# Performance work log

Measured on AMD Instinct MI355X. Metric: run time of the kernel, lower is better.

The kernel has to match this reference:

```python
import jax, jax.numpy as jnp
import numpy as np

N, E, NFEAT, HID, HEADS, NCLASS = 100000, 1600000, 256, 64, 1, 32


def gat_conv(x, src, dst, W, a_src, a_dst, b, H, C, concat):
    n = x.shape[0]
    h = (x @ W).reshape(n, H, C)                      # [N,H,C]
    a_s = (h * a_src).sum(-1)                          # [N,H]
    a_d = (h * a_dst).sum(-1)                          # [N,H]
    e = jax.nn.leaky_relu(a_s[src] + a_d[dst], 0.2)    # [E,H]
    emax = jax.ops.segment_max(e, dst, num_segments=n)
    emax = jnp.where(jnp.isfinite(emax), emax, 0.0)
    ex = jnp.exp(e - emax[dst])
    denom = jax.ops.segment_sum(ex, dst, num_segments=n)
    alpha = ex / (denom[dst] + 1e-16)                  # segment softmax over in-edges of dst
    msg = h[src] * alpha[:, :, None]                   # [E,H,C]
    out = jax.ops.segment_sum(msg, dst, num_segments=n)
    out = out.reshape(n, H * C) if concat else out.mean(axis=1)
    return out + b


def setup_inputs() -> dict:
    key = jax.random.key(0)
    ks = jax.random.split(key, 14)
    x = jax.random.normal(ks[0], (N, NFEAT), dtype=jnp.float32)
    edge_index = jax.random.randint(ks[1], (2, E), 0, N, dtype=jnp.int64)
    s = 0.05
    return {
        'x': x, 'edge_index': edge_index,
        'W1': jax.random.normal(ks[2], (NFEAT, HEADS * HID), jnp.float32) * s,
        'as1': jax.random.normal(ks[3], (HEADS, HID), jnp.float32) * s,
        'ad1': jax.random.normal(ks[4], (HEADS, HID), jnp.float32) * s,
        'b1': jnp.zeros((HEADS * HID,), jnp.float32),
        'W2': jax.random.normal(ks[5], (HEADS * HID, HEADS * HID), jnp.float32) * s,
        'as2': jax.random.normal(ks[6], (HEADS, HID), jnp.float32) * s,
        'ad2': jax.random.normal(ks[7], (HEADS, HID), jnp.float32) * s,
        'b2': jnp.zeros((HEADS * HID,), jnp.float32),
        'W3': jax.random.normal(ks[8], (HEADS * HID, HEADS * NCLASS), jnp.float32) * s,
        'as3': jax.random.normal(ks[9], (HEADS, NCLASS), jnp.float32) * s,
        'ad3': jax.random.normal(ks[10], (HEADS, NCLASS), jnp.float32) * s,
        'b3': jnp.zeros((NCLASS,), jnp.float32),
    }


def reference(x, edge_index, W1, as1, ad1, b1, W2, as2, ad2, b2, W3, as3, ad3, b3):
    # add self loops (PyG GATConv add_self_loops=True)
    loop = jnp.arange(N, dtype=edge_index.dtype)
    src = jnp.concatenate([edge_index[0], loop])
    dst = jnp.concatenate([edge_index[1], loop])
    out = jax.nn.leaky_relu(gat_conv(x, src, dst, W1, as1, ad1, b1, HEADS, HID, True), 0.01)
    out = jax.nn.leaky_relu(gat_conv(out, src, dst, W2, as2, ad2, b2, HEADS, HID, True), 0.01)
    out = gat_conv(out, src, dst, W3, as3, ad3, b3, HEADS, NCLASS, False)
    return out
```

## Files before the change

kernel.cpp:

```cpp
#include <hip/hip_runtime.h>

#define NN 100000
#define NE 1600000
#define NF 256
#define HD 64
#define NC 32

#define BKS 8
#define NBK ((NN + 255) >> 8)
#define CHUNK 4096
#define NBLK ((NE + CHUNK - 1) / CHUNK)

__device__ __forceinline__ float lrelu02(float x) { return fmaxf(x, 0.2f * x); }


__global__ __launch_bounds__(256) void bucket_hist(const int* __restrict__ dst, int* __restrict__ gcnt) {
    __shared__ int hist[NBK];
    int tid = threadIdx.x;
    for (int i = tid; i < NBK; i += 256) hist[i] = 0;
    __syncthreads();
    int base = blockIdx.x * CHUNK;
    #pragma unroll
    for (int k = 0; k < CHUNK / 256; k++) {
        int i = base + k * 256 + tid;
        if (i < NE) atomicAdd(&hist[dst[i] >> BKS], 1);
    }
    __syncthreads();
    for (int i = tid; i < NBK; i += 256) if (hist[i]) atomicAdd(&gcnt[i], hist[i]);
}

__global__ void bucket_scan(const int* __restrict__ gcnt, int* __restrict__ gbase, int* __restrict__ gcur) {
    __shared__ int sh[512];
    int tid = threadIdx.x;
    int v = (tid < NBK) ? gcnt[tid] : 0;
    sh[tid] = v;
    __syncthreads();
    for (int d = 1; d < 512; d <<= 1) {
        int t = (tid >= d) ? sh[tid - d] : 0;
        __syncthreads();
        sh[tid] += t;
        __syncthreads();
    }
    if (tid < NBK) { int ex = sh[tid] - v; gbase[tid] = ex; gcur[tid] = ex; }
}

__global__ __launch_bounds__(256) void bin_edges(const int* __restrict__ src, const int* __restrict__ dst,
                                                 int* __restrict__ gcur, int2* __restrict__ ebuf) {
    __shared__ int hist[NBK];
    __shared__ int excl[NBK];
    __shared__ int runbase[NBK];
    __shared__ int ssum[256];
    __shared__ int2 sorted[CHUNK];
    int tid = threadIdx.x;
    int base = blockIdx.x * CHUNK;
    int n = NE - base; if (n > CHUNK) n = CHUNK;

    for (int i = tid; i < NBK; i += 256) hist[i] = 0;
    __syncthreads();

    int2 ed[CHUNK / 256];
    int bk[CHUNK / 256];
    #pragma unroll
    for (int k = 0; k < CHUNK / 256; k++) {
        int i = base + k * 256 + tid;
        if (i < NE) {
            ed[k] = make_int2(src[i], dst[i]);
            bk[k] = ed[k].y >> BKS;
            atomicAdd(&hist[bk[k]], 1);
        } else bk[k] = -1;
    }
    __syncthreads();
    int h0 = (2 * tid < NBK) ? hist[2 * tid] : 0;
    int h1 = (2 * tid + 1 < NBK) ? hist[2 * tid + 1] : 0;
    ssum[tid] = h0 + h1;
    __syncthreads();
    for (int d = 1; d < 256; d <<= 1) {
        int t = (tid >= d) ? ssum[tid - d] : 0;
        __syncthreads();
        ssum[tid] += t;
        __syncthreads();
    }
    int pref = ssum[tid] - (h0 + h1);
    if (2 * tid < NBK) excl[2 * tid] = pref;
    if (2 * tid + 1 < NBK) excl[2 * tid + 1] = pref + h0;
    for (int b = tid; b < NBK; b += 256) {
        int c = hist[b];
        runbase[b] = c ? atomicAdd(&gcur[b], c) : 0;
    }
    __syncthreads();
    #pragma unroll
    for (int k = 0; k < CHUNK / 256; k++) {
        if (bk[k] >= 0) {
            int r = atomicAdd(&excl[bk[k]], 1);
            sorted[r] = ed[k];
        }
    }
    __syncthreads();
    for (int i = tid; i < n; i += 256) {
        int2 e = sorted[i];
        int b = e.y >> BKS;
        int local_rank = i - (excl[b] - hist[b]);
        ebuf[runbase[b] + local_rank] = e;
    }
}

__global__ __launch_bounds__(256) void bucket_csr(const int2* __restrict__ ebuf, const int* __restrict__ gbase,
                                                  const int* __restrict__ gcnt,
                                                  int* __restrict__ offs, int* __restrict__ csr) {
    __shared__ int hist[256], cur[256], ssum[256];
    int b = blockIdx.x, tid = threadIdx.x;
    int ebeg = gbase[b], cnt = gcnt[b];
    int node0 = b << BKS;
    hist[tid] = 0;
    __syncthreads();
    for (int i = ebeg + tid; i < ebeg + cnt; i += 256)
        atomicAdd(&hist[ebuf[i].y & 255], 1);
    __syncthreads();
    int v = hist[tid];
    ssum[tid] = v;
    __syncthreads();
    for (int d = 1; d < 256; d <<= 1) {
        int t = (tid >= d) ? ssum[tid - d] : 0;
        __syncthreads();
        ssum[tid] += t;
        __syncthreads();
    }
    int ex = ebeg + ssum[tid] - v;
    cur[tid] = ex;
    int nnode = NN - node0; if (nnode > 256) nnode = 256;
    if (tid < nnode) offs[node0 + tid] = ex;
    if (b == NBK - 1 && tid == nnode - 1) offs[NN] = ebeg + cnt;
    __syncthreads();
    for (int i = ebeg + tid; i < ebeg + cnt; i += 256) {
        int2 e = ebuf[i];
        int pos = atomicAdd(&cur[e.y & 255], 1);
        csr[pos] = e.x;
    }
}


template <int CIN, int COUT, int CG>
__global__ __launch_bounds__(256) void rb_gemm(const float* __restrict__ in, const float* __restrict__ W,
                                               const float* __restrict__ a_s, const float* __restrict__ a_d,
                                               float* __restrict__ h, float* __restrict__ asv,
                                               float* __restrict__ adv) {
    const int KC  = 32;
    const int NG  = 256 / CG;
    const int BN  = NG * 4;
    const int BNP = BN + 4;
    __shared__ float xsT[KC * BNP];
    __shared__ float Wl[KC * COUT];
    int tid = threadIdx.x;
    int cg = tid % CG;
    int ng = tid / CG;
    int c0 = cg * 8;
    int n0base = blockIdx.x * BN;

    float4 a0[4], a1[4];
    #pragma unroll
    for (int i = 0; i < 4; i++) { a0[i] = make_float4(0,0,0,0); a1[i] = make_float4(0,0,0,0); }

    for (int k0 = 0; k0 < CIN; k0 += KC) {
        __syncthreads();
        const int XF4 = BN * KC / 4;
        #pragma unroll
        for (int f = tid; f < XF4; f += 256) {
            int n = f >> 3;
            int q = f & 7;
            int gn = n0base + n;
            float4 v = make_float4(0,0,0,0);
            if (gn < NN) v = *(const float4*)&in[(size_t)gn * CIN + k0 + q * 4];
            xsT[(q * 4 + 0) * BNP + n] = v.x;
            xsT[(q * 4 + 1) * BNP + n] = v.y;
            xsT[(q * 4 + 2) * BNP + n] = v.z;
            xsT[(q * 4 + 3) * BNP + n] = v.w;
        }
        #pragma unroll
        for (int f = tid; f < KC * COUT / 4; f += 256)
            *(float4*)&Wl[f * 4] = *(const float4*)&W[(size_t)k0 * COUT + f * 4];
        __syncthreads();
        #pragma unroll 4
        for (int k = 0; k < KC; k++) {
            float4 xv = *(float4*)&xsT[k * BNP + ng * 4];
            float4 w0 = *(float4*)&Wl[k * COUT + c0];
            float4 w1 = *(float4*)&Wl[k * COUT + c0 + 4];
            #pragma unroll
            for (int i = 0; i < 4; i++) {
                float xc = (i == 0) ? xv.x : (i == 1) ? xv.y : (i == 2) ? xv.z : xv.w;
                a0[i].x += xc * w0.x; a0[i].y += xc * w0.y; a0[i].z += xc * w0.z; a0[i].w += xc * w0.w;
                a1[i].x += xc * w1.x; a1[i].y += xc * w1.y; a1[i].z += xc * w1.z; a1[i].w += xc * w1.w;
            }
        }
    }
    float4 As0 = *(const float4*)&a_s[c0];
    float4 As1 = *(const float4*)&a_s[c0 + 4];
    float4 Ad0 = *(const float4*)&a_d[c0];
    float4 Ad1 = *(const float4*)&a_d[c0 + 4];
    #pragma unroll
    for (int i = 0; i < 4; i++) {
        int n = n0base + ng * 4 + i;
        if (n < NN) {
            *(float4*)&h[(size_t)n * COUT + c0] = a0[i];
            *(float4*)&h[(size_t)n * COUT + c0 + 4] = a1[i];
        }
        float vs = a0[i].x * As0.x + a0[i].y * As0.y + a0[i].z * As0.z + a0[i].w * As0.w
                 + a1[i].x * As1.x + a1[i].y * As1.y + a1[i].z * As1.z + a1[i].w * As1.w;
        float vd = a0[i].x * Ad0.x + a0[i].y * Ad0.y + a0[i].z * Ad0.z + a0[i].w * Ad0.w
                 + a1[i].x * Ad1.x + a1[i].y * Ad1.y + a1[i].z * Ad1.z + a1[i].w * Ad1.w;
        #pragma unroll
        for (int off = 1; off < CG; off <<= 1) { vs += __shfl_xor(vs, off); vd += __shfl_xor(vd, off); }
        if (cg == 0 && n < NN) { asv[n] = vs; adv[n] = vd; }
    }
}


template <int C, bool ACT>
__global__ __launch_bounds__(256) void gat_agg(const float* __restrict__ h, const float* __restrict__ asv,
                                               const float* __restrict__ adv, const int* __restrict__ offs,
                                               const int* __restrict__ csr,
                                               const float* __restrict__ bias, float* __restrict__ out) {
    const int LPR = C / 4;
    const int G = 64 / LPR;
    const float4* h4 = (const float4*)h;
    int lane = threadIdx.x & 63;
    int v = blockIdx.x * 4 + (threadIdx.x >> 6);
    int beg = offs[v], end = offs[v + 1];
    int g = lane / LPR, r = lane % LPR;
    float adv_v = adv[v];

    float4 acc = {0.f, 0.f, 0.f, 0.f};
    float dsum = 0.f;
    #pragma unroll 4
    for (int e = beg + g; e < end; e += G) {
        int s = csr[e];
        float ww = __expf(lrelu02(asv[s] + adv_v));
        float4 hv = h4[(size_t)s * LPR + r];
        dsum += ww;
        acc.x += ww * hv.x; acc.y += ww * hv.y; acc.z += ww * hv.z; acc.w += ww * hv.w;
    }
    #pragma unroll
    for (int off = LPR; off < 64; off <<= 1) {
        acc.x += __shfl_xor(acc.x, off);
        acc.y += __shfl_xor(acc.y, off);
        acc.z += __shfl_xor(acc.z, off);
        acc.w += __shfl_xor(acc.w, off);
        dsum += __shfl_xor(dsum, off);
    }
    if (g == 0) {
        float selfw = __expf(lrelu02(asv[v] + adv_v));
        float4 hs = h4[(size_t)v * LPR + r];
        acc.x += selfw * hs.x; acc.y += selfw * hs.y;
        acc.z += selfw * hs.z; acc.w += selfw * hs.w;
        dsum += selfw;
        float inv = 1.f / (dsum + 1e-16f);
        float4 bb = ((const float4*)bias)[r];
        float4 o;
        o.x = acc.x * inv + bb.x; o.y = acc.y * inv + bb.y;
        o.z = acc.z * inv + bb.z; o.w = acc.w * inv + bb.w;
        if (ACT) {
            o.x = fmaxf(o.x, 0.01f * o.x); o.y = fmaxf(o.y, 0.01f * o.y);
            o.z = fmaxf(o.z, 0.01f * o.z); o.w = fmaxf(o.w, 0.01f * o.w);
        }
        ((float4*)out)[(size_t)v * LPR + r] = o;
    }
}


extern "C" void kernel_launch(void* const* d_in, const int* in_sizes, int n_in,
                              void* d_out, int out_size, void* d_ws, size_t ws_size,
                              hipStream_t stream) {
    const float* x   = (const float*)d_in[0];
    const int*   ei  = (const int*)d_in[1];
    const float* W1  = (const float*)d_in[2];
    const float* as1 = (const float*)d_in[3];
    const float* ad1 = (const float*)d_in[4];
    const float* b1  = (const float*)d_in[5];
    const float* W2  = (const float*)d_in[6];
    const float* as2 = (const float*)d_in[7];
    const float* ad2 = (const float*)d_in[8];
    const float* b2  = (const float*)d_in[9];
    const float* W3  = (const float*)d_in[10];
    const float* as3 = (const float*)d_in[11];
    const float* ad3 = (const float*)d_in[12];
    const float* b3  = (const float*)d_in[13];
    float* out = (float*)d_out;

    const int* srcp = ei;
    const int* dstp = ei + NE;

    char* w = (char*)d_ws;
    float* h     = (float*)w;   w += sizeof(float) * (size_t)NN * HD;
    float* featB = (float*)w;   w += sizeof(float) * (size_t)NN * HD;
    float* asv   = (float*)w;   w += sizeof(float) * NN;
    float* advv  = (float*)w;   w += sizeof(float) * NN;
    int* offs    = (int*)w;     w += sizeof(int) * (NN + 1);
    int* csr     = (int*)w;     w += sizeof(int) * (size_t)NE;
    int2* ebuf   = (int2*)w;    w += sizeof(int2) * (size_t)NE;
    int* gcnt    = (int*)w;     w += sizeof(int) * NBK;
    int* gbase   = (int*)w;     w += sizeof(int) * NBK;
    int* gcur    = (int*)w;     w += sizeof(int) * NBK;

    const int GB64 = (NN + 127) / 128;
    const int GB32 = (NN + 255) / 256;

    hipMemsetAsync(gcnt, 0, sizeof(int) * NBK, stream);
    bucket_hist<<<NBLK, 256, 0, stream>>>(dstp, gcnt);
    bucket_scan<<<1, 512, 0, stream>>>(gcnt, gbase, gcur);
    bin_edges<<<NBLK, 256, 0, stream>>>(srcp, dstp, gcur, ebuf);
    bucket_csr<<<NBK, 256, 0, stream>>>(ebuf, gbase, gcnt, offs, csr);

    rb_gemm<NF, HD, 8><<<GB64, 256, 0, stream>>>(x, W1, as1, ad1, h, asv, advv);
    gat_agg<HD, true><<<NN / 4, 256, 0, stream>>>(h, asv, advv, offs, csr, b1, featB);

    rb_gemm<HD, HD, 8><<<GB64, 256, 0, stream>>>(featB, W2, as2, ad2, h, asv, advv);
    gat_agg<HD, true><<<NN / 4, 256, 0, stream>>>(h, asv, advv, offs, csr, b2, featB);

    rb_gemm<HD, NC, 4><<<GB32, 256, 0, stream>>>(featB, W3, as3, ad3, h, asv, advv);
    gat_agg<NC, false><<<NN / 4, 256, 0, stream>>>(h, asv, advv, offs, csr, b3, out);
}
```

Baseline: 476.1 us.

## Restructure node GEMM so each wave owns a column slice with wave-uniform weight loads

The dense projection kernel is rewritten so each of the four waves handles a quarter of the output columns for 128 nodes, two nodes per lane. Weights are read directly from global memory at a wave-uniform address (readfirstlane), so they can go through scalar loads, and the shared-memory weight staging is dropped. Attention-score dot products are reduced across waves through shared memory instead of lane shuffles. The third layer now uses the same 128-node tile, which halves its per-block node count relative to before and may cost occupancy or extra launch overhead.

```diff
diff --git a/kernel.cpp b/kernel.cpp
--- a/kernel.cpp
+++ b/kernel.cpp
@@ -139,77 +139,92 @@
 }
 
 
-template <int CIN, int COUT, int CG>
-__global__ __launch_bounds__(256) void rb_gemm(const float* __restrict__ in, const float* __restrict__ W,
-                                               const float* __restrict__ a_s, const float* __restrict__ a_d,
-                                               float* __restrict__ h, float* __restrict__ asv,
-                                               float* __restrict__ adv) {
+template <int CIN, int COUT>
+__global__ __launch_bounds__(256) void rb_gemm2(const float* __restrict__ in, const float* __restrict__ W,
+                                                const float* __restrict__ a_s, const float* __restrict__ a_d,
+                                                float* __restrict__ h, float* __restrict__ asv,
+                                                float* __restrict__ adv) {
     const int KC  = 32;
-    const int NG  = 256 / CG;
-    const int BN  = NG * 4;
+    const int BN  = 128;
     const int BNP = BN + 4;
+    const int CPW = COUT / 4;
+    const int JW  = CPW / 4;
     __shared__ float xsT[KC * BNP];
-    __shared__ float Wl[KC * COUT];
-    int tid = threadIdx.x;
-    int cg = tid % CG;
-    int ng = tid / CG;
-    int c0 = cg * 8;
+    __shared__ float rs[4][BN];
+    __shared__ float rd[4][BN];
+
+    int tid  = threadIdx.x;
+    int lane = tid & 63;
+    int wave = tid >> 6;
+    int c0 = __builtin_amdgcn_readfirstlane(wave) * CPW;
     int n0base = blockIdx.x * BN;
 
-    float4 a0[4], a1[4];
-    #pragma unroll
-    for (int i = 0; i < 4; i++) { a0[i] = make_float4(0,0,0,0); a1[i] = make_float4(0,0,0,0); }
+    float4 acc[2][JW];
+    #pragma unroll
+    for (int i = 0; i < 2; i++)
+        #pragma unroll
+        for (int j = 0; j < JW; j++) acc[i][j] = make_float4(0.f, 0.f, 0.f, 0.f);
 
     for (int k0 = 0; k0 < CIN; k0 += KC) {
         __syncthreads();
-        const int XF4 = BN * KC / 4;
-        #pragma unroll
-        for (int f = tid; f < XF4; f += 256) {
+        #pragma unroll
+        for (int f = tid; f < BN * KC / 4; f += 256) {
             int n = f >> 3;
             int q = f & 7;
             int gn = n0base + n;
-            float4 v = make_float4(0,0,0,0);
+            float4 v = make_float4(0.f, 0.f, 0.f, 0.f);
             if (gn < NN) v = *(const float4*)&in[(size_t)gn * CIN + k0 + q * 4];
             xsT[(q * 4 + 0) * BNP + n] = v.x;
             xsT[(q * 4 + 1) * BNP + n] = v.y;
             xsT[(q * 4 + 2) * BNP + n] = v.z;
             xsT[(q * 4 + 3) * BNP + n] = v.w;
         }
-        #pragma unroll
-        for (int f = tid; f < KC * COUT / 4; f += 256)
-            *(float4*)&Wl[f * 4] = *(const float4*)&W[(size_t)k0 * COUT + f * 4];
-        __syncthreads();
-        #pragma unroll 4
+        __syncthreads();
+        const float* Wk = &W[(size_t)k0 * COUT + c0];
+        #pragma unroll
         for (int k = 0; k < KC; k++) {
-            float4 xv = *(float4*)&xsT[k * BNP + ng * 4];
-            float4 w0 = *(float4*)&Wl[k * COUT + c0];
-            float4 w1 = *(float4*)&Wl[k * COUT + c0 + 4];
+            float2 xv = *(const float2*)&xsT[k * BNP + (lane << 1)];
             #pragma unroll
-            for (int i = 0; i < 4; i++) {
-                float xc = (i == 0) ? xv.x : (i == 1) ? xv.y : (i == 2) ? xv.z : xv.w;
-                a0[i].x += xc * w0.x; a0[i].y += xc * w0.y; a0[i].z += xc * w0.z; a0[i].w += xc * w0.w;
-                a1[i].x += xc * w1.x; a1[i].y += xc * w1.y; a1[i].z += xc * w1.z; a1[i].w += xc * w1.w;
+            for (int j = 0; j < JW; j++) {
+                float4 wv = *(const float4*)&Wk[k * COUT + j * 4];
+                acc[0][j].x += xv.x * wv.x; acc[0][j].y += xv.x * wv.y;
+                acc[0][j].z += xv.x * wv.z; acc[0][j].w += xv.x * wv.w;
+                acc[1][j].x += xv.y * wv.x; acc[1][j].y += xv.y * wv.y;
+                acc[1][j].z += xv.y * wv.z; acc[1][j].w += xv.y * wv.w;
             }
         }
     }
-    float4 As0 = *(const float4*)&a_s[c0];
-    float4 As1 = *(const float4*)&a_s[c0 + 4];
-    float4 Ad0 = *(const float4*)&a_d[c0];
-    float4 Ad1 = *(const float4*)&a_d[c0 + 4];
-    #pragma unroll
-    for (int i = 0; i < 4; i++) {
-        int n = n0base + ng * 4 + i;
+
+    float vs0 = 0.f, vs1 = 0.f, vd0 = 0.f, vd1 = 0.f;
+    #pragma unroll
+    for (int j = 0; j < JW; j++) {
+        float4 As = *(const float4*)&a_s[c0 + j * 4];
+        float4 Ad = *(const float4*)&a_d[c0 + j * 4];
+        vs0 += acc[0][j].x * As.x + acc[0][j].y * As.y + acc[0][j].z * As.z + acc[0][j].w * As.w;
+        vs1 += acc[1][j].x * As.x + acc[1][j].y * As.y + acc[1][j].z * As.z + acc[1][j].w * As.w;
+        vd0 += acc[0][j].x * Ad.x + acc[0][j].y * Ad.y + acc[0][j].z * Ad.z + acc[0][j].w * Ad.w;
+        vd1 += acc[1][j].x * Ad.x + acc[1][j].y * Ad.y + acc[1][j].z * Ad.z + acc[1][j].w * Ad.w;
+    }
+    int n0 = n0base + (lane << 1);
+    if (n0 < NN) {
+        #pragma unroll
+        for (int j = 0; j < JW; j++) *(float4*)&h[(size_t)n0 * COUT + c0 + j * 4] = acc[0][j];
+    }
+    if (n0 + 1 < NN) {
+        #pragma unroll
+        for (int j = 0; j < JW; j++) *(float4*)&h[(size_t)(n0 + 1) * COUT + c0 + j * 4] = acc[1][j];
+    }
+    rs[wave][(lane << 1) + 0] = vs0;
+    rs[wave][(lane << 1) + 1] = vs1;
+    rd[wave][(lane << 1) + 0] = vd0;
+    rd[wave][(lane << 1) + 1] = vd1;
+    __syncthreads();
+    if (tid < BN) {
+        int n = n0base + tid;
         if (n < NN) {
-            *(float4*)&h[(size_t)n * COUT + c0] = a0[i];
-            *(float4*)&h[(size_t)n * COUT + c0 + 4] = a1[i];
-        }
-        float vs = a0[i].x * As0.x + a0[i].y * As0.y + a0[i].z * As0.z + a0[i].w * As0.w
-                 + a1[i].x * As1.x + a1[i].y * As1.y + a1[i].z * As1.z + a1[i].w * As1.w;
-        float vd = a0[i].x * Ad0.x + a0[i].y * Ad0.y + a0[i].z * Ad0.z + a0[i].w * Ad0.w
-                 + a1[i].x * Ad1.x + a1[i].y * Ad1.y + a1[i].z * Ad1.z + a1[i].w * Ad1.w;
-        #pragma unroll
-        for (int off = 1; off < CG; off <<= 1) { vs += __shfl_xor(vs, off); vd += __shfl_xor(vd, off); }
-        if (cg == 0 && n < NN) { asv[n] = vs; adv[n] = vd; }
+            asv[n] = rs[0][tid] + rs[1][tid] + rs[2][tid] + rs[3][tid];
+            adv[n] = rd[0][tid] + rd[1][tid] + rd[2][tid] + rd[3][tid];
+        }
     }
 }
 
@@ -300,8 +315,7 @@
     int* gbase   = (int*)w;     w += sizeof(int) * NBK;
     int* gcur    = (int*)w;     w += sizeof(int) * NBK;
 
-    const int GB64 = (NN + 127) / 128;
-    const int GB32 = (NN + 255) / 256;
+    const int GB = (NN + 127) / 128;
 
     hipMemsetAsync(gcnt, 0, sizeof(int) * NBK, stream);
     bucket_hist<<<NBLK, 256, 0, stream>>>(dstp, gcnt);
@@ -309,12 +323,12 @@
     bin_edges<<<NBLK, 256, 0, stream>>>(srcp, dstp, gcur, ebuf);
     bucket_csr<<<NBK, 256, 0, stream>>>(ebuf, gbase, gcnt, offs, csr);
 
-    rb_gemm<NF, HD, 8><<<GB64, 256, 0, stream>>>(x, W1, as1, ad1, h, asv, advv);
+    rb_gemm2<NF, HD><<<GB, 256, 0, stream>>>(x, W1, as1, ad1, h, asv, advv);
     gat_agg<HD, true><<<NN / 4, 256, 0, stream>>>(h, asv, advv, offs, csr, b1, featB);
 
-    rb_gemm<HD, HD, 8><<<GB64, 256, 0, stream>>>(featB, W2, as2, ad2, h, asv, advv);
+    rb_gemm2<HD, HD><<<GB, 256, 0, stream>>>(featB, W2, as2, ad2, h, asv, advv);
     gat_agg<HD, true><<<NN / 4, 256, 0, stream>>>(h, asv, advv, offs, csr, b2, featB);
 
-    rb_gemm<HD, NC, 4><<<GB32, 256, 0, stream>>>(featB, W3, as3, ad3, h, asv, advv);
+    rb_gemm2<HD, NC><<<GB, 256, 0, stream>>>(featB, W3, as3, ad3, h, asv, advv);
     gat_agg<NC, false><<<NN / 4, 256, 0, stream>>>(h, asv, advv, offs, csr, b3, out);
 }
```

After: 503.7 us. 5.8% more time.
